# Performance work log

Hardware: AMD Instinct MI355X
Metric: run time of the kernel (lower is better)

Reference implementation:

```python
import jax, jax.numpy as jnp
import numpy as np

N = 100000   # nodes
E = 1600000  # edges
D = 128      # in_channels (self and agg)
C = 128      # out_channels


def gcn_conv(x, W, b, src, dst, n):
    """PyG GCNConv: add self-loops, symmetric deg normalization, linear, scatter-add."""
    xw = x @ W  # [n, out]
    loops = jnp.arange(n)
    src2 = jnp.concatenate([src, loops])
    dst2 = jnp.concatenate([dst, loops])
    deg = jax.ops.segment_sum(jnp.ones_like(dst2, dtype=xw.dtype), dst2, num_segments=n)
    dinv = jnp.where(deg > 0, jax.lax.rsqrt(deg), 0.0)
    norm = dinv[src2] * dinv[dst2]  # [E+n]
    msg = xw[src2] * norm[:, None]  # gather + scale
    out = jax.ops.segment_sum(msg, dst2, num_segments=n)  # scatter-add at targets
    return out + b


def setup_inputs() -> dict:
    key = jax.random.key(0)
    ks = jax.random.split(key, 16)

    def w(k, shape):
        fan_in = shape[0]
        return (jax.random.uniform(k, shape, jnp.float32, -1.0, 1.0) / np.sqrt(fan_in)).astype(jnp.float32)

    inp = {
        "x_self": jax.random.normal(ks[0], (N, D), jnp.float32),
        "x_neighbor": jax.random.normal(ks[1], (N, D), jnp.float32),
        "edge_index": jax.random.randint(ks[2], (2, E), 0, N, dtype=jnp.int64),
        # linear_in_self: D -> 2C   (weights stored as [in, out])
        "W_in_self": w(ks[3], (D, 2 * C)),
        "b_in_self": w(ks[4], (2 * C,)),
        # linear_out_self: D + 2C -> C
        "W_out_self": w(ks[5], (D + 2 * C, C)),
        "b_out_self": w(ks[6], (C,)),
        # gcn1: D -> 2C ; gcn2: 2C -> C   (gcn3 unused in forward)
        "Wg1": w(ks[7], (D, 2 * C)),
        "bg1": w(ks[8], (2 * C,)),
        "Wg2": w(ks[9], (2 * C, C)),
        "bg2": w(ks[10], (C,)),
        # linear_out: D + 3C -> C
        "W_out": w(ks[11], (D + 3 * C, C)),
        "b_out": w(ks[12], (C,)),
    }
    return inp


def reference(x_self, x_neighbor, edge_index,
              W_in_self, b_in_self, W_out_self, b_out_self,
              Wg1, bg1, Wg2, bg2, W_out, b_out):
    src, dst = edge_index[0], edge_index[1]
    n = x_self.shape[0]

    # dense self branch
    l1 = jax.nn.relu(x_self @ W_in_self + b_in_self)          # [N, 2C]
    l1 = jnp.concatenate([x_self, l1], axis=1)                 # [N, D+2C]
    l1 = l1 @ W_out_self + b_out_self                          # [N, C]

    # GCN neighbor branch
    g1 = gcn_conv(x_neighbor, Wg1, bg1, src, dst, n)           # [N, 2C]
    g2 = gcn_conv(g1, Wg2, bg2, src, dst, n)                   # [N, C]
    x2 = jnp.concatenate([x_neighbor, g1, g2], axis=1)         # [N, D+3C]
    x2 = x2 @ W_out + b_out                                    # [N, C]

    return (l1, x2)
```

## Files before the change

kernel.cpp:

```cpp
#include <hip/hip_runtime.h>
#include <cstdint>
#include <cstddef>

#define NNODES 100000
#define NEDGES 1600000

typedef float f32x4 __attribute__((ext_vector_type(4)));
typedef unsigned int u32;
typedef _Float16 f16x2 __attribute__((ext_vector_type(2)));
typedef _Float16 f16x4 __attribute__((ext_vector_type(4)));
typedef _Float16 f16x8 __attribute__((ext_vector_type(8)));

__device__ __forceinline__ void gload_lds16(const void* g, void* l) {
  __builtin_amdgcn_global_load_lds((const __attribute__((address_space(1))) u32*)g,
                                   (__attribute__((address_space(3))) u32*)l, 16, 0, 0);
}


__global__ void zero_int_kernel(int* __restrict__ p, int n) {
  int i = blockIdx.x * blockDim.x + threadIdx.x;
  if (i < n) p[i] = 0;
}

__global__ void detect_kernel(const unsigned int* __restrict__ ei, int* __restrict__ flag) {
  unsigned int v = ei[2 * threadIdx.x + 1];
  unsigned long long b = __ballot(v != 0u);
  if (threadIdx.x == 0) *flag = (b == 0ull) ? 1 : 0;
}

__device__ __forceinline__ int edge_val(const void* ei, int is64, long long idx) {
  if (is64) return (int)((const long long*)ei)[idx];
  return ((const int*)ei)[idx];
}


__global__ void hist_kernel(const void* __restrict__ ei, const int* __restrict__ flag,
                            int* __restrict__ counts) {
  const int is64 = *flag;
  for (long long e = (long long)blockIdx.x * blockDim.x + threadIdx.x; e < NEDGES;
       e += (long long)gridDim.x * blockDim.x) {
    int d = edge_val(ei, is64, NEDGES + e);
    atomicAdd(&counts[d], 1);
  }
}

__global__ void dinv_kernel(const int* __restrict__ counts, float* __restrict__ dinv) {
  int i = blockIdx.x * blockDim.x + threadIdx.x;
  if (i < NNODES) dinv[i] = rsqrtf((float)(counts[i] + 1));
}

#define SCAN_B 256
#define SCAN_TILE 1024

__global__ void scan_reduce_kernel(const int* __restrict__ counts, int* __restrict__ bsums) {
  __shared__ int sd[SCAN_B];
  int t = threadIdx.x;
  int base = blockIdx.x * SCAN_TILE + t * 4;
  int s = 0;
#pragma unroll
  for (int i = 0; i < 4; i++) {
    int idx = base + i;
    if (idx < NNODES) s += counts[idx];
  }
  sd[t] = s;
  __syncthreads();
  for (int o = SCAN_B / 2; o > 0; o >>= 1) {
    if (t < o) sd[t] += sd[t + o];
    __syncthreads();
  }
  if (t == 0) bsums[blockIdx.x] = sd[0];
}

__global__ void scan_bsums_kernel(int* __restrict__ bsums, int* __restrict__ offs, int nb) {
  if (threadIdx.x == 0 && blockIdx.x == 0) {
    int run = 0;
    for (int b = 0; b < nb; b++) {
      int v = bsums[b];
      bsums[b] = run;
      run += v;
    }
    offs[NNODES] = run;
  }
}

__global__ void scan_write_kernel(const int* __restrict__ counts, const int* __restrict__ bsums,
                                  int* __restrict__ offs) {
  __shared__ int sd[SCAN_B];
  int t = threadIdx.x;
  int base = blockIdx.x * SCAN_TILE + t * 4;
  int v[4];
  int s = 0;
#pragma unroll
  for (int i = 0; i < 4; i++) {
    int idx = base + i;
    v[i] = (idx < NNODES) ? counts[idx] : 0;
    s += v[i];
  }
  sd[t] = s;
  __syncthreads();
  for (int o = 1; o < SCAN_B; o <<= 1) {
    int x = (t >= o) ? sd[t - o] : 0;
    __syncthreads();
    sd[t] += x;
    __syncthreads();
  }
  int run = sd[t] - s + bsums[blockIdx.x];
#pragma unroll
  for (int i = 0; i < 4; i++) {
    int idx = base + i;
    if (idx < NNODES) {
      offs[idx] = run;
      run += v[i];
    }
  }
}

__global__ void fill_kernel(const void* __restrict__ ei, const int* __restrict__ flag,
                            const int* __restrict__ offs, int* __restrict__ fillc,
                            int* __restrict__ csr) {
  const int is64 = *flag;
  for (long long e = (long long)blockIdx.x * blockDim.x + threadIdx.x; e < NEDGES;
       e += (long long)gridDim.x * blockDim.x) {
    int s = edge_val(ei, is64, e);
    int d = edge_val(ei, is64, NEDGES + e);
    int pos = offs[d] + atomicAdd(&fillc[d], 1);
    csr[pos] = s;
  }
}


__global__ void xcvt_kernel(const float* __restrict__ x, f16x4* __restrict__ y, int n4) {
  int i = blockIdx.x * blockDim.x + threadIdx.x;
  if (i >= n4) return;
  float4 v = ((const float4*)x)[i];
  f16x4 h;
  h[0] = (_Float16)v.x;
  h[1] = (_Float16)v.y;
  h[2] = (_Float16)v.z;
  h[3] = (_Float16)v.w;
  y[i] = h;
}


__global__ void prescale16_kernel(const f16x4* __restrict__ x, const float* __restrict__ dinv,
                                  f16x4* __restrict__ y) {
  int i = blockIdx.x * blockDim.x + threadIdx.x;
  if (i >= NNODES * 32) return;
  int row = i >> 5;
  float s = dinv[row];
  f16x4 v = x[i];
  f16x4 h;
  h[0] = (_Float16)((float)v[0] * s);
  h[1] = (_Float16)((float)v[1] * s);
  h[2] = (_Float16)((float)v[2] * s);
  h[3] = (_Float16)((float)v[3] * s);
  y[i] = h;
}


__device__ __forceinline__ float2 f16x2_to_f32(f16x2 h) {
  return make_float2((float)h[0], (float)h[1]);
}

__global__ __launch_bounds__(256) void aggregate_half_kernel(
    const f16x2* __restrict__ in, void* __restrict__ out, int out_half,
    const int* __restrict__ offs, const int* __restrict__ csr, const float* __restrict__ dinv,
    const float* __restrict__ bias) {
  int node = blockIdx.x * 4 + (threadIdx.x >> 6);
  if (node >= NNODES) return;
  int ch = threadIdx.x & 63;
  int beg = offs[node], end = offs[node + 1];

  float2 a0 = f16x2_to_f32(in[(size_t)node * 64 + ch]);
  float2 a1 = make_float2(0.f, 0.f);
  float2 a2 = make_float2(0.f, 0.f);
  float2 a3 = make_float2(0.f, 0.f);

  int p = beg;
  for (; p + 8 <= end; p += 8) {
    int j0 = csr[p + 0], j1 = csr[p + 1], j2 = csr[p + 2], j3 = csr[p + 3];
    int j4 = csr[p + 4], j5 = csr[p + 5], j6 = csr[p + 6], j7 = csr[p + 7];
    f16x2 h0 = in[(size_t)j0 * 64 + ch];
    f16x2 h1 = in[(size_t)j1 * 64 + ch];
    f16x2 h2 = in[(size_t)j2 * 64 + ch];
    f16x2 h3 = in[(size_t)j3 * 64 + ch];
    f16x2 h4 = in[(size_t)j4 * 64 + ch];
    f16x2 h5 = in[(size_t)j5 * 64 + ch];
    f16x2 h6 = in[(size_t)j6 * 64 + ch];
    f16x2 h7 = in[(size_t)j7 * 64 + ch];
    float2 v0 = f16x2_to_f32(h0);
    float2 v1 = f16x2_to_f32(h1);
    float2 v2 = f16x2_to_f32(h2);
    float2 v3 = f16x2_to_f32(h3);
    float2 v4 = f16x2_to_f32(h4);
    float2 v5 = f16x2_to_f32(h5);
    float2 v6 = f16x2_to_f32(h6);
    float2 v7 = f16x2_to_f32(h7);
    a0.x += v0.x; a0.y += v0.y;
    a1.x += v1.x; a1.y += v1.y;
    a2.x += v2.x; a2.y += v2.y;
    a3.x += v3.x; a3.y += v3.y;
    a0.x += v4.x; a0.y += v4.y;
    a1.x += v5.x; a1.y += v5.y;
    a2.x += v6.x; a2.y += v6.y;
    a3.x += v7.x; a3.y += v7.y;
  }
  for (; p + 2 <= end; p += 2) {
    int j0 = csr[p], j1 = csr[p + 1];
    float2 v0 = f16x2_to_f32(in[(size_t)j0 * 64 + ch]);
    float2 v1 = f16x2_to_f32(in[(size_t)j1 * 64 + ch]);
    a0.x += v0.x; a0.y += v0.y;
    a1.x += v1.x; a1.y += v1.y;
  }
  if (p < end) {
    float2 v0 = f16x2_to_f32(in[(size_t)csr[p] * 64 + ch]);
    a0.x += v0.x; a0.y += v0.y;
  }

  float di = dinv[node];
  int c = ch * 2;
  float2 r;
  r.x = di * (a0.x + a1.x + a2.x + a3.x);
  r.y = di * (a0.y + a1.y + a2.y + a3.y);
  if (bias) {
    r.x += bias[c];
    r.y += bias[c + 1];
  }
  if (out_half) {
    f16x2 h;
    h[0] = (_Float16)r.x;
    h[1] = (_Float16)r.y;
    ((f16x2*)out)[(size_t)node * 64 + ch] = h;
  } else {
    *(float2*)((float*)out + (size_t)node * 128 + c) = r;
  }
}


__global__ void wprep_f16_kernel(const float* __restrict__ W, int K, int M,
                                 _Float16* __restrict__ th, _Float16* __restrict__ tl) {
  int i = blockIdx.x * blockDim.x + threadIdx.x;
  if (i >= K * M) return;
  int k = i / M, m = i - k * M;
  float x = W[i];
  _Float16 h = (_Float16)x;
  th[(size_t)m * K + k] = h;
  tl[(size_t)m * K + k] = (_Float16)(x - (float)h);
}


#define BM 128
#define BN 128
#define BK 32

__global__ __launch_bounds__(256) void gemm_f16_kernel(
    const _Float16* __restrict__ A0, int K0, const _Float16* __restrict__ A1, int K1,
    const _Float16* __restrict__ A2, int K2, const _Float16* __restrict__ Bth,
    const _Float16* __restrict__ Btl, int Ktot, int M, const float* __restrict__ bias,
    const float* __restrict__ row_scale, void* __restrict__ Cmat, int relu, int out_half,
    int nrows) {
  __shared__ _Float16 As[BM * BK];
  __shared__ _Float16 Bs_h[BN * BK];
  __shared__ _Float16 Bs_l[BN * BK];

  const int tid = threadIdx.x;
  const int lane = tid & 63;
  const int wv = tid >> 6;
  const int mBase = (wv >> 1) * 64;
  const int nBase = (wv & 1) * 64;
  const int ml = lane & 15;
  const int quad = lane >> 4;
  const int rowBase = blockIdx.x * BM;
  const int colBase = blockIdx.y * BN;

  const int lrow = lane >> 2;
  const int lslot = lane & 3;

  f32x4 acc[4][4];
  const f32x4 zero = {0.f, 0.f, 0.f, 0.f};
#pragma unroll
  for (int i = 0; i < 4; i++)
#pragma unroll
    for (int j = 0; j < 4; j++) acc[i][j] = zero;

  for (int k0 = 0; k0 < Ktot; k0 += BK) {
    const _Float16* Ap;
    int kl, Kp;
    if (k0 < K0) {
      Ap = A0; kl = k0; Kp = K0;
    } else if (k0 < K0 + K1) {
      Ap = A1; kl = k0 - K0; Kp = K1;
    } else {
      Ap = A2; kl = k0 - K0 - K1; Kp = K2;
    }
#pragma unroll
    for (int c = 0; c < 2; c++) {
      int trow = wv * 32 + c * 16 + lrow;
      int sws = lslot ^ (trow & 3);
      size_t ldsoff = (size_t)(wv * 32 + c * 16) * 64;
      int gr = rowBase + trow;
      if (gr > nrows - 1) gr = nrows - 1;
      gload_lds16(Ap + (size_t)gr * Kp + kl + sws * 8, (char*)As + ldsoff);
      const _Float16* bh = Bth + (size_t)(colBase + trow) * Ktot + k0 + sws * 8;
      const _Float16* blp = Btl + (size_t)(colBase + trow) * Ktot + k0 + sws * 8;
      gload_lds16(bh, (char*)Bs_h + ldsoff);
      gload_lds16(blp, (char*)Bs_l + ldsoff);
    }
    __syncthreads();

    f16x8 av[4], bh[4], bl[4];
#pragma unroll
    for (int nt = 0; nt < 4; nt++) {
      int nrow = nBase + nt * 16 + ml;
      int boff = nrow * 32 + ((quad ^ (nrow & 3)) << 3);
      bh[nt] = *(const f16x8*)&Bs_h[boff];
      bl[nt] = *(const f16x8*)&Bs_l[boff];
    }
#pragma unroll
    for (int mt = 0; mt < 4; mt++) {
      int mrow = mBase + mt * 16 + ml;
      int aoff = mrow * 32 + ((quad ^ (mrow & 3)) << 3);
      av[mt] = *(const f16x8*)&As[aoff];
    }
#pragma unroll
    for (int mt = 0; mt < 4; mt++)
#pragma unroll
      for (int nt = 0; nt < 4; nt++) {
        acc[mt][nt] = __builtin_amdgcn_mfma_f32_16x16x32_f16(av[mt], bh[nt], acc[mt][nt], 0, 0, 0);
        acc[mt][nt] = __builtin_amdgcn_mfma_f32_16x16x32_f16(av[mt], bl[nt], acc[mt][nt], 0, 0, 0);
      }
    __syncthreads();
  }

#pragma unroll
  for (int nt = 0; nt < 4; nt++) {
    int col = colBase + nBase + nt * 16 + ml;
    float bv = bias ? bias[col] : 0.f;
#pragma unroll
    for (int mt = 0; mt < 4; mt++) {
      int row0 = rowBase + mBase + mt * 16 + quad * 4;
#pragma unroll
      for (int r = 0; r < 4; r++) {
        int grow = row0 + r;
        if (grow >= nrows) continue;
        float v = acc[mt][nt][r];
        if (row_scale) v *= row_scale[grow];
        v += bv;
        if (relu) v = fmaxf(v, 0.f);
        if (out_half) {
          ((_Float16*)Cmat)[(size_t)grow * M + col] = (_Float16)v;
        } else {
          ((float*)Cmat)[(size_t)grow * M + col] = v;
        }
      }
    }
  }
}


extern "C" void kernel_launch(void* const* d_in, const int* in_sizes, int n_in, void* d_out,
                              int out_size, void* d_ws, size_t ws_size, hipStream_t stream) {
  const float* x_self     = (const float*)d_in[0];
  const float* x_neighbor = (const float*)d_in[1];
  const void*  edge_index = d_in[2];
  const float* W_in_self  = (const float*)d_in[3];
  const float* b_in_self  = (const float*)d_in[4];
  const float* W_out_self = (const float*)d_in[5];
  const float* b_out_self = (const float*)d_in[6];
  const float* Wg1        = (const float*)d_in[7];
  const float* bg1        = (const float*)d_in[8];
  const float* Wg2        = (const float*)d_in[9];
  const float* bg2        = (const float*)d_in[10];
  const float* W_out      = (const float*)d_in[11];
  const float* b_out      = (const float*)d_in[12];
  float* out = (float*)d_out;

  char* ws = (char*)d_ws;
  size_t off = 0;
  auto alloc = [&](size_t bytes) -> void* {
    void* p = ws + off;
    off = (off + bytes + 255) & ~(size_t)255;
    return p;
  };
  int* counts = (int*)alloc((size_t)2 * NNODES * 4);
  int* fillc  = counts + NNODES;
  int*   offs   = (int*)alloc((size_t)(NNODES + 1) * 4);
  int*   csr    = (int*)alloc((size_t)NEDGES * 4);
  int*   bsums  = (int*)alloc(4096);
  int*   flag   = (int*)alloc(256);
  float* dinv   = (float*)alloc((size_t)NNODES * 4);
  _Float16* wt1h = (_Float16*)alloc(32768 * 2);
  _Float16* wt1l = (_Float16*)alloc(32768 * 2);
  _Float16* wt2h = (_Float16*)alloc(49152 * 2);
  _Float16* wt2l = (_Float16*)alloc(49152 * 2);
  _Float16* wt3h = (_Float16*)alloc(32768 * 2);
  _Float16* wt3l = (_Float16*)alloc(32768 * 2);
  _Float16* wt4h = (_Float16*)alloc(32768 * 2);
  _Float16* wt4l = (_Float16*)alloc(32768 * 2);
  _Float16* wt5h = (_Float16*)alloc(65536 * 2);
  _Float16* wt5l = (_Float16*)alloc(65536 * 2);
  float* bufA = (float*)alloc((size_t)NNODES * 256 * 4);
  float* bufB = (float*)alloc((size_t)NNODES * 256 * 4);
  (void)ws_size;

  const int nb = (NNODES + SCAN_TILE - 1) / SCAN_TILE;
  const int gridRows = (NNODES + BM - 1) / BM;

  detect_kernel<<<1, 64, 0, stream>>>((const unsigned int*)edge_index, flag);
  zero_int_kernel<<<(2 * NNODES + 255) / 256, 256, 0, stream>>>(counts, 2 * NNODES);
  hist_kernel<<<1024, 256, 0, stream>>>(edge_index, flag, counts);
  dinv_kernel<<<(NNODES + 255) / 256, 256, 0, stream>>>(counts, dinv);
  scan_reduce_kernel<<<nb, SCAN_B, 0, stream>>>(counts, bsums);
  scan_bsums_kernel<<<1, 64, 0, stream>>>(bsums, offs, nb);
  scan_write_kernel<<<nb, SCAN_B, 0, stream>>>(counts, bsums, offs);
  fill_kernel<<<1024, 256, 0, stream>>>(edge_index, flag, offs, fillc, csr);

  wprep_f16_kernel<<<(32768 + 255) / 256, 256, 0, stream>>>(W_in_self, 128, 256, wt1h, wt1l);
  wprep_f16_kernel<<<(49152 + 255) / 256, 256, 0, stream>>>(W_out_self, 384, 128, wt2h, wt2l);
  wprep_f16_kernel<<<(32768 + 255) / 256, 256, 0, stream>>>(Wg1, 128, 256, wt3h, wt3l);
  wprep_f16_kernel<<<(32768 + 255) / 256, 256, 0, stream>>>(Wg2, 256, 128, wt4h, wt4l);
  wprep_f16_kernel<<<(65536 + 255) / 256, 256, 0, stream>>>(W_out, 512, 128, wt5h, wt5l);

  _Float16* xs16 = (_Float16*)(bufB + (size_t)NNODES * 128);
  _Float16* xn16 = xs16 + (size_t)NNODES * 128;
  xcvt_kernel<<<(NNODES * 32 + 255) / 256, 256, 0, stream>>>(x_self, (f16x4*)xs16, NNODES * 32);
  xcvt_kernel<<<(NNODES * 32 + 255) / 256, 256, 0, stream>>>(x_neighbor, (f16x4*)xn16,
                                                             NNODES * 32);

  _Float16* l1 = (_Float16*)bufA;
  gemm_f16_kernel<<<dim3(gridRows, 2), 256, 0, stream>>>(
      xs16, 128, nullptr, 0, nullptr, 0, wt1h, wt1l, 128, 256, b_in_self, nullptr, l1, 1, 1,
      NNODES);
  gemm_f16_kernel<<<dim3(gridRows, 1), 256, 0, stream>>>(
      xs16, 128, l1, 256, nullptr, 0, wt2h, wt2l, 384, 128, b_out_self, nullptr, out, 0, 0,
      NNODES);

  _Float16* ybuf = (_Float16*)bufB;
  _Float16* aggx = (_Float16*)bufA;
  _Float16* g1   = (_Float16*)bufB;
  _Float16* xw2  = (_Float16*)bufA;
  _Float16* g2   = (_Float16*)bufA + (size_t)NNODES * 128;

  prescale16_kernel<<<(NNODES * 32 + 255) / 256, 256, 0, stream>>>((const f16x4*)xn16, dinv,
                                                                   (f16x4*)ybuf);
  aggregate_half_kernel<<<NNODES / 4, 256, 0, stream>>>((const f16x2*)ybuf, aggx, 1, offs, csr,
                                                        dinv, nullptr);
  gemm_f16_kernel<<<dim3(gridRows, 2), 256, 0, stream>>>(
      aggx, 128, nullptr, 0, nullptr, 0, wt3h, wt3l, 128, 256, bg1, nullptr, g1, 0, 1, NNODES);
  gemm_f16_kernel<<<dim3(gridRows, 1), 256, 0, stream>>>(
      g1, 256, nullptr, 0, nullptr, 0, wt4h, wt4l, 256, 128, nullptr, dinv, xw2, 0, 1, NNODES);
  aggregate_half_kernel<<<NNODES / 4, 256, 0, stream>>>((const f16x2*)xw2, g2, 1, offs, csr,
                                                        dinv, bg2);
  gemm_f16_kernel<<<dim3(gridRows, 1), 256, 0, stream>>>(
      xn16, 128, g1, 256, g2, 128, wt5h, wt5l, 512, 128, b_out, nullptr,
      out + (size_t)NNODES * 128, 0, 0, NNODES);
}
```

Before: 788.8 us.

## Build CSR via two-pass bucketing with LDS-window scatter

```diff
diff --git a/kernel.cpp b/kernel.cpp
--- a/kernel.cpp
+++ b/kernel.cpp
@@ -115,16 +115,86 @@
   }
 }
 
-__global__ void fill_kernel(const void* __restrict__ ei, const int* __restrict__ flag,
-                            const int* __restrict__ offs, int* __restrict__ fillc,
-                            int* __restrict__ csr) {
+
+#define BK_SHIFT 8
+#define NBUCK 391
+#define BCAP 8192
+#define WCAP 12288
+
+__global__ __launch_bounds__(256) void bucket_kernel(
+    const void* __restrict__ ei, const int* __restrict__ flag, const int* __restrict__ offs,
+    int* __restrict__ fillc, int* __restrict__ gcount,
+    unsigned long long* __restrict__ bpairs, int* __restrict__ csr) {
+  __shared__ int lcount[NBUCK];
+  __shared__ int gbase[NBUCK];
+  __shared__ int lcur[NBUCK];
   const int is64 = *flag;
-  for (long long e = (long long)blockIdx.x * blockDim.x + threadIdx.x; e < NEDGES;
-       e += (long long)gridDim.x * blockDim.x) {
+  const int chunk = NEDGES / 256;
+  const long long e0 = (long long)blockIdx.x * chunk;
+  const long long e1 = e0 + chunk;
+  for (int i = threadIdx.x; i < NBUCK; i += 256) {
+    lcount[i] = 0;
+    lcur[i] = 0;
+  }
+  __syncthreads();
+  for (long long e = e0 + threadIdx.x; e < e1; e += 256) {
+    int d = edge_val(ei, is64, NEDGES + e);
+    atomicAdd(&lcount[d >> BK_SHIFT], 1);
+  }
+  __syncthreads();
+  for (int i = threadIdx.x; i < NBUCK; i += 256) {
+    int c = lcount[i];
+    gbase[i] = c ? atomicAdd(&gcount[i], c) : 0;
+  }
+  __syncthreads();
+  for (long long e = e0 + threadIdx.x; e < e1; e += 256) {
     int s = edge_val(ei, is64, e);
     int d = edge_val(ei, is64, NEDGES + e);
-    int pos = offs[d] + atomicAdd(&fillc[d], 1);
-    csr[pos] = s;
+    int b = d >> BK_SHIFT;
+    int pos = gbase[b] + atomicAdd(&lcur[b], 1);
+    if (pos < BCAP) {
+      bpairs[(size_t)b * BCAP + pos] =
+          ((unsigned long long)(unsigned)d << 32) | (unsigned)s;
+    } else {
+      int p = offs[d] + atomicAdd(&fillc[d], 1);
+      csr[p] = s;
+    }
+  }
+}
+
+__global__ __launch_bounds__(256) void fillwin_kernel(
+    const unsigned long long* __restrict__ bpairs, const int* __restrict__ gcount,
+    const int* __restrict__ offs, int* __restrict__ fillc, int* __restrict__ csr) {
+  __shared__ int win[WCAP];
+  __shared__ int nfill[256];
+  const int b = blockIdx.x;
+  const int nlo = b << BK_SHIFT;
+  const int nhi = min(nlo + 256, NNODES);
+  const int base = offs[nlo];
+  const int W = offs[nhi] - base;
+  int cnt = gcount[b];
+  if (cnt > BCAP) cnt = BCAP;
+  if (W <= WCAP) {
+    if ((int)threadIdx.x < nhi - nlo) nfill[threadIdx.x] = fillc[nlo + threadIdx.x];
+    for (int i = threadIdx.x; i < W; i += 256) win[i] = csr[base + i];
+    __syncthreads();
+    for (int i = threadIdx.x; i < cnt; i += 256) {
+      unsigned long long v = bpairs[(size_t)b * BCAP + i];
+      int d = (int)(v >> 32);
+      int s = (int)(v & 0xffffffffull);
+      int p = offs[d] - base + atomicAdd(&nfill[d - nlo], 1);
+      win[p] = s;
+    }
+    __syncthreads();
+    for (int i = threadIdx.x; i < W; i += 256) csr[base + i] = win[i];
+  } else {
+    for (int i = threadIdx.x; i < cnt; i += 256) {
+      unsigned long long v = bpairs[(size_t)b * BCAP + i];
+      int d = (int)(v >> 32);
+      int s = (int)(v & 0xffffffffull);
+      int p = offs[d] + atomicAdd(&fillc[d], 1);
+      csr[p] = s;
+    }
   }
 }
 
@@ -382,8 +452,9 @@
     off = (off + bytes + 255) & ~(size_t)255;
     return p;
   };
-  int* counts = (int*)alloc((size_t)2 * NNODES * 4);
+  int* counts = (int*)alloc((size_t)2 * NNODES * 4 + 2048);
   int* fillc  = counts + NNODES;
+  int* gcount = counts + 2 * NNODES;
   int*   offs   = (int*)alloc((size_t)(NNODES + 1) * 4);
   int*   csr    = (int*)alloc((size_t)NEDGES * 4);
   int*   bsums  = (int*)alloc(4096);
@@ -403,17 +474,21 @@
   float* bufB = (float*)alloc((size_t)NNODES * 256 * 4);
   (void)ws_size;
 
+  unsigned long long* bpairs = (unsigned long long*)bufA;
+
   const int nb = (NNODES + SCAN_TILE - 1) / SCAN_TILE;
   const int gridRows = (NNODES + BM - 1) / BM;
 
   detect_kernel<<<1, 64, 0, stream>>>((const unsigned int*)edge_index, flag);
-  zero_int_kernel<<<(2 * NNODES + 255) / 256, 256, 0, stream>>>(counts, 2 * NNODES);
+  zero_int_kernel<<<(2 * NNODES + 512 + 255) / 256, 256, 0, stream>>>(counts,
+                                                                      2 * NNODES + 512);
   hist_kernel<<<1024, 256, 0, stream>>>(edge_index, flag, counts);
   dinv_kernel<<<(NNODES + 255) / 256, 256, 0, stream>>>(counts, dinv);
   scan_reduce_kernel<<<nb, SCAN_B, 0, stream>>>(counts, bsums);
   scan_bsums_kernel<<<1, 64, 0, stream>>>(bsums, offs, nb);
   scan_write_kernel<<<nb, SCAN_B, 0, stream>>>(counts, bsums, offs);
-  fill_kernel<<<1024, 256, 0, stream>>>(edge_index, flag, offs, fillc, csr);
+  bucket_kernel<<<256, 256, 0, stream>>>(edge_index, flag, offs, fillc, gcount, bpairs, csr);
+  fillwin_kernel<<<NBUCK, 256, 0, stream>>>(bpairs, gcount, offs, fillc, csr);
 
   wprep_f16_kernel<<<(32768 + 255) / 256, 256, 0, stream>>>(W_in_self, 128, 256, wt1h, wt1l);
   wprep_f16_kernel<<<(49152 + 255) / 256, 256, 0, stream>>>(W_out_self, 384, 128, wt2h, wt2l);
```

Result: faster. 760.9 us (-3.5%).
